# Kernel tuning notes

Measured on AMD Instinct MI355X. Metric: run time of the kernel, lower is better.

Reference implementation:

```python
import jax, jax.numpy as jnp
import numpy as np

WS = 7       # window size
SHIFT = 3    # shift size (ws//2)
NH = 16      # num heads
DIM = 512    # channels
HH = 112
WW = 112
HIDDEN = int(DIM * 4.0)
EPS = 1e-5


def _rel_index():
    # Swin relative position index, [N, N] ints into the bias table
    coords = np.stack(np.meshgrid(np.arange(WS), np.arange(WS), indexing='ij')).reshape(2, -1)
    rel = coords[:, :, None] - coords[:, None, :]
    rel = rel.transpose(1, 2, 0) + (WS - 1)
    rel[:, :, 0] *= 2 * WS - 1
    return rel.sum(-1)


def _attn_mask():
    # shifted-window mask on HH x WW (already multiples of WS) -> [nW, N, N] with 0 / -1e9
    img = np.zeros((HH, WW), np.int32)
    cnt = 0
    sl = (slice(0, -WS), slice(-WS, -SHIFT), slice(-SHIFT, None))
    for h in sl:
        for w in sl:
            img[h, w] = cnt
            cnt += 1
    win = img.reshape(HH // WS, WS, WW // WS, WS).transpose(0, 2, 1, 3).reshape(-1, WS * WS)
    diff = win[:, None, :] - win[:, :, None]
    return np.where(diff == 0, 0.0, -1e9).astype(np.float32)


def setup_inputs() -> dict:
    key = jax.random.key(0)
    ks = jax.random.split(key, 8)
    s = 0.02
    return {
        'x': jax.random.normal(ks[0], (DIM, HH, WW), jnp.float32),
        'norm1_w': jnp.ones((DIM,), jnp.float32),
        'norm1_b': jnp.zeros((DIM,), jnp.float32),
        'qkv_w': jax.random.normal(ks[1], (3 * DIM, DIM), jnp.float32) * s,
        'qkv_b': jnp.zeros((3 * DIM,), jnp.float32),
        'proj_w': jax.random.normal(ks[2], (DIM, DIM), jnp.float32) * s,
        'proj_b': jnp.zeros((DIM,), jnp.float32),
        'rpb_table': jax.random.normal(ks[3], ((2 * WS - 1) ** 2, NH), jnp.float32) * s,
        'norm2_w': jnp.ones((DIM,), jnp.float32),
        'norm2_b': jnp.zeros((DIM,), jnp.float32),
        'fc1_w': jax.random.normal(ks[4], (HIDDEN, DIM), jnp.float32) * s,
        'fc1_b': jnp.zeros((HIDDEN,), jnp.float32),
        'fc2_w': jax.random.normal(ks[5], (DIM, HIDDEN), jnp.float32) * s,
        'fc2_b': jnp.zeros((DIM,), jnp.float32),
    }


def _ln(x_hwc, w, b):
    m = x_hwc.mean(-1, keepdims=True)
    v = x_hwc.var(-1, keepdims=True)
    return (x_hwc - m) / jnp.sqrt(v + EPS) * w + b


def reference(x, norm1_w, norm1_b, qkv_w, qkv_b, proj_w, proj_b, rpb_table,
              norm2_w, norm2_b, fc1_w, fc1_b, fc2_w, fc2_b):
    C, H, W = x.shape
    ws = WS
    N = ws * ws
    hd = C // NH
    scale = 1.0 / np.sqrt(hd).astype(np.float32)

    x_hwc = jnp.moveaxis(x, 0, -1)                       # [H,W,C]
    xn = _ln(x_hwc, norm1_w, norm1_b)
    xs = jnp.roll(xn, (-SHIFT, -SHIFT), (0, 1))          # cyclic shift
    # window partition -> [nW, N, C]
    xw = xs.reshape(H // ws, ws, W // ws, ws, C).transpose(0, 2, 1, 3, 4).reshape(-1, N, C)

    qkv = xw @ qkv_w.T + qkv_b                            # [nW,N,3C]
    q, k, v = jnp.split(qkv, 3, -1)
    heads = lambda t: t.reshape(-1, N, NH, hd).transpose(0, 2, 1, 3)  # [nW,H,N,hd]
    q, k, v = heads(q), heads(k), heads(v)

    attn = jnp.einsum('whnd,whmd->whnm', q * scale, k)    # [nW,H,N,N]
    idx = jnp.asarray(_rel_index().reshape(-1))
    bias = rpb_table[idx].reshape(N, N, NH).transpose(2, 0, 1)  # [H,N,N]
    mask = jnp.asarray(_attn_mask())                       # [nW,N,N]
    attn = attn + bias[None] + mask[:, None]
    attn = jax.nn.softmax(attn, -1)

    out = jnp.einsum('whnm,whmd->whnd', attn, v).transpose(0, 2, 1, 3).reshape(-1, N, C)
    out = out @ proj_w.T + proj_b
    # window unpartition + reverse shift
    out = out.reshape(H // ws, W // ws, ws, ws, C).transpose(0, 2, 1, 3, 4).reshape(H, W, C)
    out = jnp.roll(out, (SHIFT, SHIFT), (0, 1))

    x1 = x_hwc + out                                       # residual (DropPath rate 0)
    x2 = _ln(x1, norm2_w, norm2_b)
    h = jax.nn.gelu(x2.reshape(-1, C) @ fc1_w.T + fc1_b)
    m = (h @ fc2_w.T + fc2_b).reshape(H, W, C)
    y = x1 + m
    return jnp.moveaxis(y, -1, 0)                          # back to [C,H,W]
```

## Files before the change

kernel.cpp:

```cpp
#include <hip/hip_runtime.h>

#define NPIX 12544
#define CDIM 512
#define QKVN 1536
#define HIDDEN 2048

typedef unsigned short u16;
typedef unsigned int u32;

typedef short bf16x8 __attribute__((ext_vector_type(8)));
typedef float f32x4 __attribute__((ext_vector_type(4)));

static __device__ __forceinline__ u16 f2bf(float f) {
  u32 u = __float_as_uint(f);
  return (u16)((u + 0x7fffu + ((u >> 16) & 1u)) >> 16);
}
static __device__ __forceinline__ u32 pack2(float a, float b) {
  return (u32)f2bf(a) | ((u32)f2bf(b) << 16);
}
static __device__ __forceinline__ u32 packtrunc2(float lo, float hi) {
  return __builtin_amdgcn_perm(__float_as_uint(hi), __float_as_uint(lo), 0x07060302u);
}
static __device__ __forceinline__ void async_ld16(const void* g, void* l) {
  __builtin_amdgcn_global_load_lds((__attribute__((address_space(1))) void*)g,
                                   (__attribute__((address_space(3))) void*)l, 16, 0, 0);
}

__global__ __launch_bounds__(256) void convert_weights(
    const float* __restrict__ qw, const float* __restrict__ pw,
    const float* __restrict__ w1, const float* __restrict__ w2,
    u16* __restrict__ Wq, u16* __restrict__ Wp, u16* __restrict__ W1o, u16* __restrict__ W2o) {
  const int b = blockIdx.x;
  const float* src; u16* dst; long off;
  if (b < 768)       { src = qw; dst = Wq;  off = (long)b * 1024; }
  else if (b < 1024) { src = pw; dst = Wp;  off = (long)(b - 768) * 1024; }
  else if (b < 2048) { src = w1; dst = W1o; off = (long)(b - 1024) * 1024; }
  else               { src = w2; dst = W2o; off = (long)(b - 2048) * 1024; }
  const long i = off / 4 + threadIdx.x;
  const float4 v = ((const float4*)src)[i];
  ushort4 u;
  u.x = f2bf(v.x); u.y = f2bf(v.y); u.z = f2bf(v.z); u.w = f2bf(v.w);
  ((ushort4*)dst)[i] = u;
}

__global__ __launch_bounds__(256) void ln1_partial(const float* __restrict__ x,
                                                   float* __restrict__ psum, float* __restrict__ pssq) {
  const int p = blockIdx.x * 256 + threadIdx.x;
  const int c0 = blockIdx.y * 32;
  float s = 0.f, ss = 0.f;
#pragma unroll
  for (int c = 0; c < 32; c++) {
    const float v = x[(long)(c0 + c) * NPIX + p];
    s += v; ss += v * v;
  }
  psum[blockIdx.y * NPIX + p] = s;
  pssq[blockIdx.y * NPIX + p] = ss;
}

__global__ __launch_bounds__(256) void ln1_stats(const float* __restrict__ psum, const float* __restrict__ pssq,
                                                 float* __restrict__ mean, float* __restrict__ rstd) {
  const int p = blockIdx.x * 256 + threadIdx.x;
  float s = 0.f, ss = 0.f;
#pragma unroll
  for (int ch = 0; ch < 16; ch++) { s += psum[ch * NPIX + p]; ss += pssq[ch * NPIX + p]; }
  const float m = s * (1.f / 512.f);
  const float v = ss * (1.f / 512.f) - m * m;
  mean[p] = m;
  rstd[p] = rsqrtf(v + 1e-5f);
}

__global__ __launch_bounds__(256) void ln1_shift_part(const float* __restrict__ x,
    const float* __restrict__ mean, const float* __restrict__ rstd,
    const float* __restrict__ gw, const float* __restrict__ gb, u16* __restrict__ xw) {
  __shared__ float tile[32][65];
  const int p0 = blockIdx.x * 64;
  const int c0 = blockIdx.y * 32;
  const int t = threadIdx.x;
  {
    const int pl = t & 63;
    const int cl0 = t >> 6;
#pragma unroll
    for (int r = 0; r < 8; r++) {
      const int cl = r * 4 + cl0;
      tile[cl][pl] = x[(long)(c0 + cl) * NPIX + p0 + pl];
    }
  }
  __syncthreads();
  const int cl = t & 31;
  const int g = t >> 5;
  const float wc = gw[c0 + cl];
  const float bc = gb[c0 + cl];
#pragma unroll
  for (int pass = 0; pass < 8; pass++) {
    const int pl = pass * 8 + g;
    const int p = p0 + pl;
    const int h = p / 112;
    const int w = p - h * 112;
    int hs = h + 109; if (hs >= 112) hs -= 112;
    int ws2 = w + 109; if (ws2 >= 112) ws2 -= 112;
    const int hq = hs / 7, wq = ws2 / 7;
    const int tok = (hq * 16 + wq) * 49 + (hs - hq * 7) * 7 + (ws2 - wq * 7);
    const float val = (tile[cl][pl] - mean[p]) * rstd[p] * wc + bc;
    xw[(long)tok * 512 + c0 + cl] = f2bf(val);
  }
}

template<bool OUT_BF16, bool DO_GELU, bool REMAP, bool FUSE_Y, bool FUSE_X>
__global__ __launch_bounds__(256, 3) void gemm_bt(
    const u16* __restrict__ A, const u16* __restrict__ B,
    const float* __restrict__ bias, void* __restrict__ out,
    const float* __restrict__ xtra, const int N, const int K) {
  __shared__ __align__(16) u16 Asm[2][128 * 32];
  __shared__ __align__(16) u16 Bsm[2][128 * 32];
  const int M0 = blockIdx.x << 7;
  const int N0 = blockIdx.y << 7;
  const int t = threadIdx.x;
  const int wave = t >> 6;
  const int lane = t & 63;
  const int l15 = lane & 15;
  const int quad = lane >> 4;
  const int wm = wave & 1;
  const int wn = wave >> 1;
  const int swz = (l15 >> 1) & 3;

  auto stage = [&](int k0, int b) {
#pragma unroll
    for (int i = 0; i < 2; i++) {
      const int flatbase = i * 256 + wave * 64;
      const int FL = flatbase + lane;
      const int row = FL >> 2;
      const int chunk = (FL & 3) ^ ((row >> 1) & 3);
      async_ld16(A + (long)(M0 + row) * K + k0 + chunk * 8, &Asm[b][flatbase * 8]);
      async_ld16(B + (long)(N0 + row) * K + k0 + chunk * 8, &Bsm[b][flatbase * 8]);
    }
  };

  f32x4 acc[4][4] = {};
  stage(0, 0);
  int cur = 0;

  for (int k0 = 0; k0 < K; k0 += 32) {
    __syncthreads();
    if (k0 + 32 < K) stage(k0 + 32, cur ^ 1);
    bf16x8 af[4], bfr[4];
#pragma unroll
    for (int im = 0; im < 4; im++)
      af[im] = *(const bf16x8*)&Asm[cur][(wm * 64 + im * 16 + l15) * 32 + (quad ^ swz) * 8];
#pragma unroll
    for (int in = 0; in < 4; in++)
      bfr[in] = *(const bf16x8*)&Bsm[cur][(wn * 64 + in * 16 + l15) * 32 + (quad ^ swz) * 8];
#pragma unroll
    for (int im = 0; im < 4; im++)
#pragma unroll
      for (int in = 0; in < 4; in++)
        acc[im][in] = __builtin_amdgcn_mfma_f32_16x16x32_bf16(bfr[in], af[im], acc[im][in], 0, 0, 0);
    cur ^= 1;
  }

#pragma unroll
  for (int im = 0; im < 4; im++) {
    const int row = M0 + wm * 64 + im * 16 + l15;
    long orow = row;
    if (REMAP) {
      const int win = row / 49;
      const int nn = row - win * 49;
      const int nq = nn / 7;
      const int hs = (win >> 4) * 7 + nq;
      const int wsx = (win & 15) * 7 + (nn - nq * 7);
      int h = hs + 3; if (h >= 112) h -= 112;
      int w = wsx + 3; if (w >= 112) w -= 112;
      orow = h * 112 + w;
    }
#pragma unroll
    for (int in = 0; in < 4; in++) {
      const int col0 = N0 + wn * 64 + in * 16 + quad * 4;
      const float4 bv = *(const float4*)(bias + col0);
      float v[4];
      if (FUSE_Y) {
        const float4 xv = *(const float4*)(xtra + (long)row * CDIM + col0);
#pragma unroll
        for (int r = 0; r < 4; r++)
          v[r] = acc[im][in][r] + ((const float*)&bv)[r] + ((const float*)&xv)[r];
#pragma unroll
        for (int r = 0; r < 4; r++)
          ((float*)out)[(long)(col0 + r) * NPIX + row] = v[r];
      } else if (FUSE_X) {
        float v0 = acc[im][in][0] + bv.x + xtra[(long)(col0 + 0) * NPIX + orow];
        float v1 = acc[im][in][1] + bv.y + xtra[(long)(col0 + 1) * NPIX + orow];
        float v2 = acc[im][in][2] + bv.z + xtra[(long)(col0 + 2) * NPIX + orow];
        float v3 = acc[im][in][3] + bv.w + xtra[(long)(col0 + 3) * NPIX + orow];
        float4 f; f.x = v0; f.y = v1; f.z = v2; f.w = v3;
        *(float4*)((float*)out + orow * (long)N + col0) = f;
      } else {
#pragma unroll
        for (int r = 0; r < 4; r++) {
          float vv = acc[im][in][r] + ((const float*)&bv)[r];
          if (DO_GELU) {
            const float z2 = 1.5957691216f * (vv + 0.044715f * vv * vv * vv);
            vv = vv / (1.0f + __expf(-z2));
          }
          v[r] = vv;
        }
        if (OUT_BF16) {
          uint2 u;
          u.x = pack2(v[0], v[1]);
          u.y = pack2(v[2], v[3]);
          *(uint2*)((u16*)out + orow * (long)N + col0) = u;
        } else {
          float4 f; f.x = v[0]; f.y = v[1]; f.z = v[2]; f.w = v[3];
          *(float4*)((float*)out + orow * (long)N + col0) = f;
        }
      }
    }
  }
}

__global__ __launch_bounds__(256) void build_biasT(const float* __restrict__ rpb, float* __restrict__ biasT) {
  const int cls = blockIdx.x >> 4;
  const int head = blockIdx.x & 15;
  for (int e = threadIdx.x; e < 4096; e += 256) {
    const int j = e >> 6;
    const int i = e & 63;
    float v;
    if (j >= 49) v = -1e9f;
    else if (i >= 49) v = 0.f;
    else {
      const int ri = i / 7, ci = i - (i / 7) * 7;
      const int rj = j / 7, cj = j - (j / 7) * 7;
      v = rpb[((ri - rj + 6) * 13 + (ci - cj + 6)) * 16 + head];
      const int lhi = (cls & 2) ? (ri < 4 ? 1 : 2) : 0;
      const int lwi = (cls & 1) ? (ci < 4 ? 1 : 2) : 0;
      const int lhj = (cls & 2) ? (rj < 4 ? 1 : 2) : 0;
      const int lwj = (cls & 1) ? (cj < 4 ? 1 : 2) : 0;
      if (lhi * 3 + lwi != lhj * 3 + lwj) v = -1e9f;
    }
    biasT[(long)blockIdx.x * 4096 + e] = v;
  }
}

__global__ __launch_bounds__(256, 3) void attn_mfma(
    const u16* __restrict__ qkv, const float* __restrict__ biasT, u16* __restrict__ out) {
  __shared__ __align__(16) u16 slds[24576];
  const int t = threadIdx.x;
  const int wave = t >> 6;
  const int lane = t & 63;
  const int l15 = lane & 15;
  const int quad = lane >> 4;
  const int win = blockIdx.x >> 2;
  const int head = (blockIdx.x & 3) * 4 + wave;
  const int cls = (((win >> 4) == 15) ? 2 : 0) | (((win & 15) == 15) ? 1 : 0);

  u16* Qb  = slds + wave * 6144;
  u16* Kb  = Qb + 2048;
  u16* Vtb = Qb + 4096;
  u16* Pb  = Qb;

  const int rrow = lane >> 2;
  const int chunk = (lane & 3) ^ ((lane >> 3) & 3);
  uint4 vv[4];
#pragma unroll
  for (int it = 0; it < 4; it++) {
    const int row = it * 16 + rrow;
    const int jc = row < 49 ? row : 48;
    const long gbase = (long)(win * 49 + jc) * 1536 + head * 32 + chunk * 8;
    async_ld16(qkv + gbase,       Qb + it * 512 + lane * 8);
    async_ld16(qkv + gbase + 512, Kb + it * 512 + lane * 8);
    vv[it] = *(const uint4*)(qkv + gbase + 1024);
  }
  __syncthreads();

#pragma unroll
  for (int it = 0; it < 4; it++) {
    const int row = it * 16 + rrow;
    const u32* w = (const u32*)&vv[it];
#pragma unroll
    for (int tt = 0; tt < 8; tt++) {
      const int d = chunk * 8 + tt;
      const u16 val = (tt & 1) ? (u16)(w[tt >> 1] >> 16) : (u16)(w[tt >> 1] & 0xffffu);
      Vtb[d * 64 + (row ^ (((d >> 2) & 3) << 4))] = val;
    }
  }

  const int fswz = (l15 >> 1) & 3;
  bf16x8 kfrag[4], qfrag[4];
#pragma unroll
  for (int jm = 0; jm < 4; jm++)
    kfrag[jm] = *(const bf16x8*)(Kb + (jm * 16 + l15) * 32 + (quad ^ fswz) * 8);
#pragma unroll
  for (int in = 0; in < 4; in++)
    qfrag[in] = *(const bf16x8*)(Qb + (in * 16 + l15) * 32 + (quad ^ fswz) * 8);
  f32x4 sacc[4][4] = {};
#pragma unroll
  for (int jm = 0; jm < 4; jm++)
#pragma unroll
    for (int in = 0; in < 4; in++)
      sacc[jm][in] = __builtin_amdgcn_mfma_f32_16x16x32_bf16(kfrag[jm], qfrag[in], sacc[jm][in], 0, 0, 0);

  const float* bT = biasT + (long)(cls * 16 + head) * 4096;
  const float sc = 0.17677669529663687f;
#pragma unroll
  for (int jm = 0; jm < 4; jm++) {
    const float* bp = bT + (jm * 16 + quad * 4) * 64 + l15;
#pragma unroll
    for (int in = 0; in < 4; in++)
#pragma unroll
      for (int r = 0; r < 4; r++)
        sacc[jm][in][r] = sacc[jm][in][r] * sc + bp[r * 64 + in * 16];
  }
  float linv[4];
#pragma unroll
  for (int in = 0; in < 4; in++) {
    float m = -1e30f;
#pragma unroll
    for (int jm = 0; jm < 4; jm++)
#pragma unroll
      for (int r = 0; r < 4; r++) m = fmaxf(m, sacc[jm][in][r]);
    m = fmaxf(m, __shfl_xor(m, 16));
    m = fmaxf(m, __shfl_xor(m, 32));
    float s = 0.f;
#pragma unroll
    for (int jm = 0; jm < 4; jm++)
#pragma unroll
      for (int r = 0; r < 4; r++) {
        const float e = __expf(sacc[jm][in][r] - m);
        sacc[jm][in][r] = e; s += e;
      }
    s += __shfl_xor(s, 16);
    s += __shfl_xor(s, 32);
    linv[in] = __builtin_amdgcn_rcpf(s);
  }

#pragma unroll
  for (int in = 0; in < 4; in++) {
    const int i = in * 16 + l15;
    const int rot = (l15 & 3) << 4;
#pragma unroll
    for (int jm = 0; jm < 4; jm++) {
      const u32 lo = packtrunc2(sacc[jm][in][0], sacc[jm][in][1]);
      const u32 hi = packtrunc2(sacc[jm][in][2], sacc[jm][in][3]);
      uint2 u; u.x = lo; u.y = hi;
      *(uint2*)(Pb + i * 64 + ((jm * 16 + quad * 4) ^ rot)) = u;
    }
  }

  f32x4 oacc[2][4] = {};
#pragma unroll
  for (int ks = 0; ks < 2; ks++) {
    bf16x8 vtf[2], pf[4];
#pragma unroll
    for (int dm = 0; dm < 2; dm++)
      vtf[dm] = *(const bf16x8*)(Vtb + (dm * 16 + l15) * 64 + ((ks * 32 + quad * 8) ^ ((l15 >> 2) << 4)));
#pragma unroll
    for (int in = 0; in < 4; in++)
      pf[in] = *(const bf16x8*)(Pb + (in * 16 + l15) * 64 + ((ks * 32 + quad * 8) ^ ((l15 & 3) << 4)));
#pragma unroll
    for (int dm = 0; dm < 2; dm++)
#pragma unroll
      for (int in = 0; in < 4; in++)
        oacc[dm][in] = __builtin_amdgcn_mfma_f32_16x16x32_bf16(vtf[dm], pf[in], oacc[dm][in], 0, 0, 0);
  }

#pragma unroll
  for (int in = 0; in < 4; in++) {
    const int i = in * 16 + l15;
    if (i < 49) {
      const float inv = linv[in];
      const long base = (long)(win * 49 + i) * 512 + head * 32 + quad * 4;
#pragma unroll
      for (int dm = 0; dm < 2; dm++) {
        const float v0 = oacc[dm][in][0] * inv, v1 = oacc[dm][in][1] * inv;
        const float v2 = oacc[dm][in][2] * inv, v3 = oacc[dm][in][3] * inv;
        uint2 u; u.x = packtrunc2(v0, v1); u.y = packtrunc2(v2, v3);
        *(uint2*)(out + base + dm * 16) = u;
      }
    }
  }
}

__global__ __launch_bounds__(256) void ln2_apply(const float* __restrict__ x1,
    const float* __restrict__ gw, const float* __restrict__ gb, u16* __restrict__ x2) {
  const int wave = threadIdx.x >> 6;
  const int lane = threadIdx.x & 63;
  const int p = blockIdx.x * 4 + wave;
  const float4* row = (const float4*)(x1 + (long)p * 512);
  const float4 a = row[lane * 2];
  const float4 b = row[lane * 2 + 1];
  float s = a.x + a.y + a.z + a.w + b.x + b.y + b.z + b.w;
  float ss = a.x * a.x + a.y * a.y + a.z * a.z + a.w * a.w
           + b.x * b.x + b.y * b.y + b.z * b.z + b.w * b.w;
#pragma unroll
  for (int o = 32; o > 0; o >>= 1) { s += __shfl_xor(s, o); ss += __shfl_xor(ss, o); }
  const float m = s * (1.f / 512.f);
  const float var = ss * (1.f / 512.f) - m * m;
  const float rs = rsqrtf(var + 1e-5f);
  const float4 w0 = ((const float4*)gw)[lane * 2];
  const float4 w1 = ((const float4*)gw)[lane * 2 + 1];
  const float4 b0 = ((const float4*)gb)[lane * 2];
  const float4 b1 = ((const float4*)gb)[lane * 2 + 1];
  uint4 u;
  u.x = pack2((a.x - m) * rs * w0.x + b0.x, (a.y - m) * rs * w0.y + b0.y);
  u.y = pack2((a.z - m) * rs * w0.z + b0.z, (a.w - m) * rs * w0.w + b0.w);
  u.z = pack2((b.x - m) * rs * w1.x + b1.x, (b.y - m) * rs * w1.y + b1.y);
  u.w = pack2((b.z - m) * rs * w1.z + b1.z, (b.w - m) * rs * w1.w + b1.w);
  ((uint4*)(x2 + (long)p * 512))[lane] = u;
}

extern "C" void kernel_launch(void* const* d_in, const int* in_sizes, int n_in,
                              void* d_out, int out_size, void* d_ws, size_t ws_size,
                              hipStream_t stream) {
  (void)in_sizes; (void)n_in; (void)out_size; (void)ws_size;
  const float* x      = (const float*)d_in[0];
  const float* n1w    = (const float*)d_in[1];
  const float* n1b    = (const float*)d_in[2];
  const float* qkv_w  = (const float*)d_in[3];
  const float* qkv_b  = (const float*)d_in[4];
  const float* proj_w = (const float*)d_in[5];
  const float* proj_b = (const float*)d_in[6];
  const float* rpb    = (const float*)d_in[7];
  const float* n2w    = (const float*)d_in[8];
  const float* n2b    = (const float*)d_in[9];
  const float* fc1_w  = (const float*)d_in[10];
  const float* fc1_b  = (const float*)d_in[11];
  const float* fc2_w  = (const float*)d_in[12];
  const float* fc2_b  = (const float*)d_in[13];
  float* y = (float*)d_out;

  char* base = (char*)d_ws;
  size_t off = 0;
  auto alloc = [&](size_t b) { char* p = base + off; off += (b + 255) & ~(size_t)255; return p; };
  float* mean1 = (float*)alloc((size_t)NPIX * 4);
  float* rstd1 = (float*)alloc((size_t)NPIX * 4);
  float* psum  = (float*)alloc((size_t)16 * NPIX * 4);
  float* pssq  = (float*)alloc((size_t)16 * NPIX * 4);
  u16* Wq = (u16*)alloc((size_t)QKVN * CDIM * 2);
  u16* Wp = (u16*)alloc((size_t)CDIM * CDIM * 2);
  u16* W1 = (u16*)alloc((size_t)HIDDEN * CDIM * 2);
  u16* W2 = (u16*)alloc((size_t)CDIM * HIDDEN * 2);
  float* biasT = (float*)alloc((size_t)4 * 16 * 4096 * 4);
  u16* bufA = (u16*)alloc((size_t)NPIX * CDIM * 2);
  char* bufB = alloc((size_t)NPIX * QKVN * 2);
  float* x1 = (float*)alloc((size_t)NPIX * CDIM * 4);
  u16* hbuf = (u16*)alloc((size_t)NPIX * HIDDEN * 2);

  u16* xw      = bufA;
  u16* qkvbuf  = (u16*)bufB;
  u16* attnout = bufA;
  u16* x2 = bufA;

  convert_weights<<<3072, 256, 0, stream>>>(qkv_w, proj_w, fc1_w, fc2_w, Wq, Wp, W1, W2);
  build_biasT<<<64, 256, 0, stream>>>(rpb, biasT);

  ln1_partial<<<dim3(49, 16), 256, 0, stream>>>(x, psum, pssq);
  ln1_stats<<<49, 256, 0, stream>>>(psum, pssq, mean1, rstd1);
  ln1_shift_part<<<dim3(196, 16), 256, 0, stream>>>(x, mean1, rstd1, n1w, n1b, xw);

  gemm_bt<true, false, false, false, false><<<dim3(98, QKVN / 128), 256, 0, stream>>>(xw, Wq, qkv_b, qkvbuf, nullptr, QKVN, CDIM);
  attn_mfma<<<1024, 256, 0, stream>>>(qkvbuf, biasT, attnout);
  gemm_bt<false, false, true, false, true><<<dim3(98, CDIM / 128), 256, 0, stream>>>(attnout, Wp, proj_b, x1, x, CDIM, CDIM);

  ln2_apply<<<NPIX / 4, 256, 0, stream>>>(x1, n2w, n2b, x2);

  gemm_bt<true, true, false, false, false><<<dim3(98, HIDDEN / 128), 256, 0, stream>>>(x2, W1, fc1_b, hbuf, nullptr, HIDDEN, CDIM);
  gemm_bt<false, false, false, true, false><<<dim3(98, CDIM / 128), 256, 0, stream>>>(hbuf, W2, fc2_b, y, x1, CDIM, HIDDEN);
}
```

Measured before the change: 327.1 us.

## Replace LDS-staged GEMM with single-wave register-direct 64x64 tile GEMM

Rewrites the shared GEMM kernel so that each 64-thread block computes a 64x64 output tile. Operands are loaded directly from global memory into registers with double buffering, replacing the 256-thread 128x128 tile with async global-to-LDS staging. K becomes a template parameter, so the K loop is fully unrolled. This removes LDS traffic and barrier syncs, but lowers operand reuse per tile and increases global/L2 traffic and per-lane strided loads.

```diff
diff --git a/kernel.cpp b/kernel.cpp
--- a/kernel.cpp
+++ b/kernel.cpp
@@ -105,61 +105,48 @@
   }
 }
 
-template<bool OUT_BF16, bool DO_GELU, bool REMAP, bool FUSE_Y, bool FUSE_X>
-__global__ __launch_bounds__(256, 3) void gemm_bt(
+template<bool OUT_BF16, bool DO_GELU, bool REMAP, bool FUSE_Y, bool FUSE_X, int K>
+__global__ __launch_bounds__(64, 3) void gemm_rf(
     const u16* __restrict__ A, const u16* __restrict__ B,
     const float* __restrict__ bias, void* __restrict__ out,
-    const float* __restrict__ xtra, const int N, const int K) {
-  __shared__ __align__(16) u16 Asm[2][128 * 32];
-  __shared__ __align__(16) u16 Bsm[2][128 * 32];
-  const int M0 = blockIdx.x << 7;
-  const int N0 = blockIdx.y << 7;
-  const int t = threadIdx.x;
-  const int wave = t >> 6;
-  const int lane = t & 63;
+    const float* __restrict__ xtra, const int N) {
+  const int M0 = blockIdx.y << 6;
+  const int N0 = blockIdx.x << 6;
+  const int lane = threadIdx.x;
   const int l15 = lane & 15;
   const int quad = lane >> 4;
-  const int wm = wave & 1;
-  const int wn = wave >> 1;
-  const int swz = (l15 >> 1) & 3;
-
-  auto stage = [&](int k0, int b) {
-#pragma unroll
-    for (int i = 0; i < 2; i++) {
-      const int flatbase = i * 256 + wave * 64;
-      const int FL = flatbase + lane;
-      const int row = FL >> 2;
-      const int chunk = (FL & 3) ^ ((row >> 1) & 3);
-      async_ld16(A + (long)(M0 + row) * K + k0 + chunk * 8, &Asm[b][flatbase * 8]);
-      async_ld16(B + (long)(N0 + row) * K + k0 + chunk * 8, &Bsm[b][flatbase * 8]);
-    }
-  };
+
+  const u16* Ap = A + (long)(M0 + l15) * K + quad * 8;
+  const u16* Bp = B + (long)(N0 + l15) * K + quad * 8;
 
   f32x4 acc[4][4] = {};
-  stage(0, 0);
-  int cur = 0;
-
-  for (int k0 = 0; k0 < K; k0 += 32) {
-    __syncthreads();
-    if (k0 + 32 < K) stage(k0 + 32, cur ^ 1);
-    bf16x8 af[4], bfr[4];
+  bf16x8 af[2][4], bfr[2][4];
+
+#pragma unroll
+  for (int im = 0; im < 4; im++) af[0][im] = *(const bf16x8*)(Ap + (long)im * 16 * K);
+#pragma unroll
+  for (int in = 0; in < 4; in++) bfr[0][in] = *(const bf16x8*)(Bp + (long)in * 16 * K);
+
+#pragma unroll
+  for (int ks = 0; ks < K / 32; ks++) {
+    const int cur = ks & 1;
+    if (ks + 1 < K / 32) {
+      const int k = (ks + 1) * 32;
+#pragma unroll
+      for (int im = 0; im < 4; im++) af[cur ^ 1][im] = *(const bf16x8*)(Ap + (long)im * 16 * K + k);
+#pragma unroll
+      for (int in = 0; in < 4; in++) bfr[cur ^ 1][in] = *(const bf16x8*)(Bp + (long)in * 16 * K + k);
+    }
 #pragma unroll
     for (int im = 0; im < 4; im++)
-      af[im] = *(const bf16x8*)&Asm[cur][(wm * 64 + im * 16 + l15) * 32 + (quad ^ swz) * 8];
-#pragma unroll
-    for (int in = 0; in < 4; in++)
-      bfr[in] = *(const bf16x8*)&Bsm[cur][(wn * 64 + in * 16 + l15) * 32 + (quad ^ swz) * 8];
-#pragma unroll
-    for (int im = 0; im < 4; im++)
 #pragma unroll
       for (int in = 0; in < 4; in++)
-        acc[im][in] = __builtin_amdgcn_mfma_f32_16x16x32_bf16(bfr[in], af[im], acc[im][in], 0, 0, 0);
-    cur ^= 1;
+        acc[im][in] = __builtin_amdgcn_mfma_f32_16x16x32_bf16(bfr[cur][in], af[cur][im], acc[im][in], 0, 0, 0);
   }
 
 #pragma unroll
   for (int im = 0; im < 4; im++) {
-    const int row = M0 + wm * 64 + im * 16 + l15;
+    const int row = M0 + im * 16 + l15;
     long orow = row;
     if (REMAP) {
       const int win = row / 49;
@@ -173,7 +160,7 @@
     }
 #pragma unroll
     for (int in = 0; in < 4; in++) {
-      const int col0 = N0 + wn * 64 + in * 16 + quad * 4;
+      const int col0 = N0 + in * 16 + quad * 4;
       const float4 bv = *(const float4*)(bias + col0);
       float v[4];
       if (FUSE_Y) {
@@ -454,12 +441,12 @@
   ln1_stats<<<49, 256, 0, stream>>>(psum, pssq, mean1, rstd1);
   ln1_shift_part<<<dim3(196, 16), 256, 0, stream>>>(x, mean1, rstd1, n1w, n1b, xw);
 
-  gemm_bt<true, false, false, false, false><<<dim3(98, QKVN / 128), 256, 0, stream>>>(xw, Wq, qkv_b, qkvbuf, nullptr, QKVN, CDIM);
+  gemm_rf<true, false, false, false, false, CDIM><<<dim3(QKVN / 64, 196), 64, 0, stream>>>(xw, Wq, qkv_b, qkvbuf, nullptr, QKVN);
   attn_mfma<<<1024, 256, 0, stream>>>(qkvbuf, biasT, attnout);
-  gemm_bt<false, false, true, false, true><<<dim3(98, CDIM / 128), 256, 0, stream>>>(attnout, Wp, proj_b, x1, x, CDIM, CDIM);
+  gemm_rf<false, false, true, false, true, CDIM><<<dim3(CDIM / 64, 196), 64, 0, stream>>>(attnout, Wp, proj_b, x1, x, CDIM);
 
   ln2_apply<<<NPIX / 4, 256, 0, stream>>>(x1, n2w, n2b, x2);
 
-  gemm_bt<true, true, false, false, false><<<dim3(98, HIDDEN / 128), 256, 0, stream>>>(x2, W1, fc1_b, hbuf, nullptr, HIDDEN, CDIM);
-  gemm_bt<false, false, false, true, false><<<dim3(98, CDIM / 128), 256, 0, stream>>>(hbuf, W2, fc2_b, y, x1, CDIM, HIDDEN);
-}
+  gemm_rf<true, true, false, false, false, CDIM><<<dim3(HIDDEN / 64, 196), 64, 0, stream>>>(x2, W1, fc1_b, hbuf, nullptr, HIDDEN);
+  gemm_rf<false, false, false, true, false, HIDDEN><<<dim3(CDIM / 64, 196), 64, 0, stream>>>(hbuf, W2, fc2_b, y, x1, CDIM);
+}
```

Measured after the change: 495.9 us. 1.52x slower.

## Single-buffer GEMM LDS staging and swap grid axes for N-major block order

Applied to the files above, without the earlier changes.

Replaces the double-buffered LDS prefetch in the GEMM kernel with a single buffer: each K step loads the tile, syncs, computes, then syncs again. It also swaps the grid dimensions so blocks sharing the same A row-tile are launched consecutively, aiming for better L2 reuse of activations. Halving LDS may allow more resident blocks, but it removes the overlap between global loads and MFMA work and adds a barrier per iteration.

```diff
diff --git a/kernel.cpp b/kernel.cpp
--- a/kernel.cpp
+++ b/kernel.cpp
@@ -110,10 +110,10 @@
     const u16* __restrict__ A, const u16* __restrict__ B,
     const float* __restrict__ bias, void* __restrict__ out,
     const float* __restrict__ xtra, const int N, const int K) {
-  __shared__ __align__(16) u16 Asm[2][128 * 32];
-  __shared__ __align__(16) u16 Bsm[2][128 * 32];
-  const int M0 = blockIdx.x << 7;
-  const int N0 = blockIdx.y << 7;
+  __shared__ __align__(16) u16 Asm[128 * 32];
+  __shared__ __align__(16) u16 Bsm[128 * 32];
+  const int M0 = blockIdx.y << 7;
+  const int N0 = blockIdx.x << 7;
   const int t = threadIdx.x;
   const int wave = t >> 6;
   const int lane = t & 63;
@@ -123,38 +123,32 @@
   const int wn = wave >> 1;
   const int swz = (l15 >> 1) & 3;
 
-  auto stage = [&](int k0, int b) {
+  f32x4 acc[4][4] = {};
+
+  for (int k0 = 0; k0 < K; k0 += 32) {
 #pragma unroll
     for (int i = 0; i < 2; i++) {
       const int flatbase = i * 256 + wave * 64;
       const int FL = flatbase + lane;
       const int row = FL >> 2;
       const int chunk = (FL & 3) ^ ((row >> 1) & 3);
-      async_ld16(A + (long)(M0 + row) * K + k0 + chunk * 8, &Asm[b][flatbase * 8]);
-      async_ld16(B + (long)(N0 + row) * K + k0 + chunk * 8, &Bsm[b][flatbase * 8]);
-    }
-  };
-
-  f32x4 acc[4][4] = {};
-  stage(0, 0);
-  int cur = 0;
-
-  for (int k0 = 0; k0 < K; k0 += 32) {
+      async_ld16(A + (long)(M0 + row) * K + k0 + chunk * 8, &Asm[flatbase * 8]);
+      async_ld16(B + (long)(N0 + row) * K + k0 + chunk * 8, &Bsm[flatbase * 8]);
+    }
     __syncthreads();
-    if (k0 + 32 < K) stage(k0 + 32, cur ^ 1);
     bf16x8 af[4], bfr[4];
 #pragma unroll
     for (int im = 0; im < 4; im++)
-      af[im] = *(const bf16x8*)&Asm[cur][(wm * 64 + im * 16 + l15) * 32 + (quad ^ swz) * 8];
+      af[im] = *(const bf16x8*)&Asm[(wm * 64 + im * 16 + l15) * 32 + (quad ^ swz) * 8];
 #pragma unroll
     for (int in = 0; in < 4; in++)
-      bfr[in] = *(const bf16x8*)&Bsm[cur][(wn * 64 + in * 16 + l15) * 32 + (quad ^ swz) * 8];
+      bfr[in] = *(const bf16x8*)&Bsm[(wn * 64 + in * 16 + l15) * 32 + (quad ^ swz) * 8];
 #pragma unroll
     for (int im = 0; im < 4; im++)
 #pragma unroll
       for (int in = 0; in < 4; in++)
         acc[im][in] = __builtin_amdgcn_mfma_f32_16x16x32_bf16(bfr[in], af[im], acc[im][in], 0, 0, 0);
-    cur ^= 1;
+    __syncthreads();
   }
 
 #pragma unroll
@@ -454,12 +448,12 @@
   ln1_stats<<<49, 256, 0, stream>>>(psum, pssq, mean1, rstd1);
   ln1_shift_part<<<dim3(196, 16), 256, 0, stream>>>(x, mean1, rstd1, n1w, n1b, xw);
 
-  gemm_bt<true, false, false, false, false><<<dim3(98, QKVN / 128), 256, 0, stream>>>(xw, Wq, qkv_b, qkvbuf, nullptr, QKVN, CDIM);
+  gemm_bt<true, false, false, false, false><<<dim3(QKVN / 128, 98), 256, 0, stream>>>(xw, Wq, qkv_b, qkvbuf, nullptr, QKVN, CDIM);
   attn_mfma<<<1024, 256, 0, stream>>>(qkvbuf, biasT, attnout);
-  gemm_bt<false, false, true, false, true><<<dim3(98, CDIM / 128), 256, 0, stream>>>(attnout, Wp, proj_b, x1, x, CDIM, CDIM);
+  gemm_bt<false, false, true, false, true><<<dim3(CDIM / 128, 98), 256, 0, stream>>>(attnout, Wp, proj_b, x1, x, CDIM, CDIM);
 
   ln2_apply<<<NPIX / 4, 256, 0, stream>>>(x1, n2w, n2b, x2);
 
-  gemm_bt<true, true, false, false, false><<<dim3(98, HIDDEN / 128), 256, 0, stream>>>(x2, W1, fc1_b, hbuf, nullptr, HIDDEN, CDIM);
-  gemm_bt<false, false, false, true, false><<<dim3(98, CDIM / 128), 256, 0, stream>>>(hbuf, W2, fc2_b, y, x1, CDIM, HIDDEN);
-}
+  gemm_bt<true, true, false, false, false><<<dim3(HIDDEN / 128, 98), 256, 0, stream>>>(x2, W1, fc1_b, hbuf, nullptr, HIDDEN, CDIM);
+  gemm_bt<false, false, false, true, false><<<dim3(CDIM / 128, 98), 256, 0, stream>>>(hbuf, W2, fc2_b, y, x1, CDIM, HIDDEN);
+}
```

After: 317.2 us. 1.03x faster.
